# Kernel optimization log

Measured on AMD Instinct MI355X. Metric: run time of the kernel, lower is better.

Reference implementation:

```python
import jax, jax.numpy as jnp
import numpy as np

B, N, VDIM = 64, 256, 2048
LRDIM, EMBED = 64, 1024


def setup_inputs() -> dict:
    key = jax.random.key(0)
    ks = jax.random.split(key, 12)
    s = 1.0 / np.sqrt(VDIM)
    return {
        "Vmat": jax.random.normal(ks[0], (B, N, VDIM), dtype=jnp.float32),
        # weight-normed linear_U1: W = g * v / ||v||_row, bias b
        "U1_v": jax.random.normal(ks[1], (LRDIM, VDIM), dtype=jnp.float32) * s,
        "U1_g": jax.random.uniform(ks[2], (LRDIM,), dtype=jnp.float32, minval=0.5, maxval=1.5),
        "U1_b": jax.random.normal(ks[3], (LRDIM,), dtype=jnp.float32) * s,
        "U2_v": jax.random.normal(ks[4], (LRDIM, VDIM), dtype=jnp.float32) * s,
        "U2_g": jax.random.uniform(ks[5], (LRDIM,), dtype=jnp.float32, minval=0.5, maxval=1.5),
        "U2_b": jax.random.normal(ks[6], (LRDIM,), dtype=jnp.float32) * s,
        # final projection + BatchNorm1d affine params
        "W_lin": jax.random.normal(ks[7], (EMBED, VDIM), dtype=jnp.float32) * s,
        "b_lin": jax.random.normal(ks[8], (EMBED,), dtype=jnp.float32) * s,
        "bn_gamma": jnp.ones((EMBED,), dtype=jnp.float32),
        "bn_beta": jnp.zeros((EMBED,), dtype=jnp.float32),
    }


def _weight_norm(v, g):
    # torch weight_norm with dim=0: per output row
    return v * (g / jnp.linalg.norm(v, axis=1))[:, None]


def reference(Vmat, U1_v, U1_g, U1_b, U2_v, U2_g, U2_b, W_lin, b_lin, bn_gamma, bn_beta):
    # forward(Vmat, t_method='uncorr', model_num=6) -> UnCorrVmat_Detail path
    W1 = _weight_norm(U1_v, U1_g)
    W2 = _weight_norm(U2_v, U2_g)
    right = jax.nn.relu(jnp.einsum('bnv,kv->bnk', Vmat, W1) + U1_b)   # [B,N,LR]
    left = jax.nn.relu(jnp.einsum('bnv,kv->bnk', Vmat, W2) + U2_b)    # [B,N,LR]
    uncorr = jnp.einsum('bnk,bmk->bnm', left, right)                   # [B,N,N]
    # vectorized per-batch diag rsqrt normalization
    d = jax.lax.rsqrt(jnp.einsum('bii->bi', uncorr) + 1e-6)            # [B,N]
    uncorr = d[:, None, :] * uncorr * d[:, :, None]
    uncorr = 1.0 + jnp.eye(Vmat.shape[1], dtype=Vmat.dtype) - uncorr
    feats = jnp.mean(jnp.einsum('bnm,bmv->bnv', uncorr, Vmat), axis=1)  # [B,VDIM]
    # linear + BatchNorm1d (training mode: biased batch stats)
    x = feats @ W_lin.T + b_lin                                        # [B,EMBED]
    mu = jnp.mean(x, axis=0)
    var = jnp.mean(jnp.square(x - mu), axis=0)
    return bn_gamma * (x - mu) * jax.lax.rsqrt(var + 1e-5) + bn_beta
```

## Files before the change

kernel.cpp:

```cpp
#include <hip/hip_runtime.h>

#define B_ 64
#define N_ 256
#define V_ 2048
#define E_ 1024
#define MROWS 16384

typedef __bf16 bf16_t;
typedef bf16_t bf16x8 __attribute__((ext_vector_type(8)));
typedef float f32x4 __attribute__((ext_vector_type(4)));

#define OFF_LR  16384
#define OFF_FT  2113536
#define FTSZ    131072
#define OFF_WB  2637824

__device__ __forceinline__ void gload_lds16(const bf16_t* g, bf16_t* l) {
    __builtin_amdgcn_global_load_lds((const __attribute__((address_space(1))) void*)g,
                                     (__attribute__((address_space(3))) void*)l, 16, 0, 0);
}

__global__ void kprep(const float* __restrict__ U1v, const float* __restrict__ U1g,
                      const float* __restrict__ U2v, const float* __restrict__ U2g,
                      bf16_t* __restrict__ Wb) {
    __shared__ float red[256];
    __shared__ float sc;
    const int r = blockIdx.x;
    const float* v = (r < 64) ? (U1v + (size_t)r * V_) : (U2v + (size_t)(r - 64) * V_);
    float ss = 0.f;
    for (int i = threadIdx.x; i < V_; i += 256) { float x = v[i]; ss += x * x; }
    red[threadIdx.x] = ss;
    __syncthreads();
    for (int o = 128; o > 0; o >>= 1) {
        if (threadIdx.x < (unsigned)o) red[threadIdx.x] += red[threadIdx.x + o];
        __syncthreads();
    }
    if (threadIdx.x == 0) {
        float g = (r < 64) ? U1g[r] : U2g[r - 64];
        sc = g * rsqrtf(red[0]);
    }
    __syncthreads();
    const float s = sc;
    const int k = threadIdx.x * 8;
    float4 f0 = *(const float4*)(v + k);
    float4 f1 = *(const float4*)(v + k + 4);
    bf16x8 o;
    o[0] = (bf16_t)(f0.x * s); o[1] = (bf16_t)(f0.y * s);
    o[2] = (bf16_t)(f0.z * s); o[3] = (bf16_t)(f0.w * s);
    o[4] = (bf16_t)(f1.x * s); o[5] = (bf16_t)(f1.y * s);
    o[6] = (bf16_t)(f1.z * s); o[7] = (bf16_t)(f1.w * s);
    *(bf16x8*)(Wb + (size_t)r * V_ + k) = o;
}

#define BK 128
__global__ __launch_bounds__(256) void gemm_lr(
    const float* __restrict__ V, const bf16_t* __restrict__ Wb,
    const float* __restrict__ U1b, const float* __restrict__ U2b,
    float* __restrict__ LR) {
    __shared__ bf16_t As[32 * BK];
    __shared__ bf16_t Bs[128 * BK];
    const int t = threadIdx.x;
    const int m0 = blockIdx.x * 32;
    const int wv = t >> 6, lane = t & 63;
    const int lm = lane & 15, lq = lane >> 4;
    const int n0w = wv * 32;

    const int ar = t >> 3, au = t & 7;
    const float* aptr = V + (size_t)(m0 + ar) * V_ + au * 8;
    bf16_t* adst0 = &As[ar * BK + ((au ^ (ar & 15)) * 8)];
    bf16_t* adst1 = &As[ar * BK + (((au + 8) ^ (ar & 15)) * 8)];

    const int rloc = lane >> 4, cc = lane & 15;
    const int r15 = wv * 4 + rloc;
    const bf16_t* bgsrc = Wb + (size_t)r15 * V_ + (cc ^ r15) * 8;

    f32x4 acc[2][2];
#pragma unroll
    for (int i = 0; i < 2; ++i)
#pragma unroll
        for (int j = 0; j < 2; ++j) acc[i][j] = (f32x4){0.f, 0.f, 0.f, 0.f};

#pragma unroll
    for (int q = 0; q < 8; ++q)
        gload_lds16(bgsrc + (size_t)q * 16 * V_, &Bs[(q * 16 + wv * 4) * BK]);
    float4 ap0 = *(const float4*)(aptr);
    float4 ap1 = *(const float4*)(aptr + 4);
    float4 ap2 = *(const float4*)(aptr + 64);
    float4 ap3 = *(const float4*)(aptr + 68);

    for (int k0 = 0; k0 < V_; k0 += BK) {
        bf16x8 av0, av1;
        av0[0] = (bf16_t)ap0.x; av0[1] = (bf16_t)ap0.y; av0[2] = (bf16_t)ap0.z; av0[3] = (bf16_t)ap0.w;
        av0[4] = (bf16_t)ap1.x; av0[5] = (bf16_t)ap1.y; av0[6] = (bf16_t)ap1.z; av0[7] = (bf16_t)ap1.w;
        av1[0] = (bf16_t)ap2.x; av1[1] = (bf16_t)ap2.y; av1[2] = (bf16_t)ap2.z; av1[3] = (bf16_t)ap2.w;
        av1[4] = (bf16_t)ap3.x; av1[5] = (bf16_t)ap3.y; av1[6] = (bf16_t)ap3.z; av1[7] = (bf16_t)ap3.w;
        *(bf16x8*)adst0 = av0;
        *(bf16x8*)adst1 = av1;
        __syncthreads();

#pragma unroll
        for (int h = 0; h < 2; ++h) {
            bf16x8 af[2][2], bfr[2][2];
#pragma unroll
            for (int i = 0; i < 2; ++i)
#pragma unroll
                for (int kf = 0; kf < 2; ++kf)
                    af[i][kf] = *(bf16x8*)&As[(i * 16 + lm) * BK + ((((h * 2 + kf) * 4 + lq) ^ lm) * 8)];
#pragma unroll
            for (int j = 0; j < 2; ++j)
#pragma unroll
                for (int kf = 0; kf < 2; ++kf)
                    bfr[j][kf] = *(bf16x8*)&Bs[(n0w + j * 16 + lm) * BK + ((((h * 2 + kf) * 4 + lq) ^ lm) * 8)];
            if (h == 1 && k0 + BK < V_) {
                ap0 = *(const float4*)(aptr + k0 + BK);
                ap1 = *(const float4*)(aptr + k0 + BK + 4);
                ap2 = *(const float4*)(aptr + k0 + BK + 64);
                ap3 = *(const float4*)(aptr + k0 + BK + 68);
            }
#pragma unroll
            for (int i = 0; i < 2; ++i)
#pragma unroll
                for (int j = 0; j < 2; ++j) {
                    acc[i][j] = __builtin_amdgcn_mfma_f32_16x16x32_bf16(af[i][0], bfr[j][0], acc[i][j], 0, 0, 0);
                    acc[i][j] = __builtin_amdgcn_mfma_f32_16x16x32_bf16(af[i][1], bfr[j][1], acc[i][j], 0, 0, 0);
                }
        }
        __syncthreads();
        if (k0 + BK < V_) {
#pragma unroll
            for (int q = 0; q < 8; ++q)
                gload_lds16(bgsrc + (size_t)q * 16 * V_ + (k0 + BK), &Bs[(q * 16 + wv * 4) * BK]);
        }
    }
#pragma unroll
    for (int j = 0; j < 2; ++j) {
        const int n = n0w + j * 16 + lm;
        const float bi = (n < 64) ? U1b[n] : U2b[n - 64];
#pragma unroll
        for (int i = 0; i < 2; ++i)
#pragma unroll
            for (int r = 0; r < 4; ++r) {
                const int m = m0 + i * 16 + lq * 4 + r;
                LR[(size_t)m * 128 + n] = fmaxf(acc[i][j][r] + bi, 0.f);
            }
    }
}

__global__ __launch_bounds__(256) void kfs(const float* __restrict__ LR,
                                           const float* __restrict__ Vmat,
                                           float* __restrict__ F) {
    const int b = blockIdx.x >> 2, vc = blockIdx.x & 3;
    const float* Lb = LR + (size_t)b * N_ * 128;
    __shared__ float dl[256];
    __shared__ float red[4][64];
    __shared__ float lbar[64];
    __shared__ float sl[256];
    __shared__ float4 part[256];
    const int t = threadIdx.x;
    const float* row = Lb + (size_t)t * 128;
    float dd = 0.f;
#pragma unroll
    for (int k = 0; k < 64; k += 4) {
        float4 l = *(const float4*)(row + k);
        float4 r = *(const float4*)(row + 64 + k);
        dd += l.x * r.x + l.y * r.y + l.z * r.z + l.w * r.w;
    }
    const float dv = rsqrtf(dd + 1e-6f);
    dl[t] = dv;
    __syncthreads();
    const int k = t & 63, g = t >> 6;
    float acc = 0.f;
    for (int n = g; n < N_; n += 4)
        acc += dl[n] * Lb[(size_t)n * 128 + 64 + k];
    red[g][k] = acc;
    __syncthreads();
    if (t < 64) lbar[t] = red[0][t] + red[1][t] + red[2][t] + red[3][t];
    __syncthreads();
    float a2 = 0.f;
#pragma unroll 8
    for (int kk = 0; kk < 64; ++kk) a2 += lbar[kk] * row[kk];
    sl[t] = ((float)(N_ + 1) - dv * a2) * (1.0f / (float)N_);
    __syncthreads();
    const int v4 = t & 127, mh = t >> 7;
    const int v = vc * 512 + v4 * 4;
    const float* base = Vmat + (size_t)b * N_ * V_ + (size_t)mh * 128 * V_ + v;
    float4 a = {0.f, 0.f, 0.f, 0.f};
    for (int m = 0; m < 128; m += 16) {
        float4 x[16];
#pragma unroll
        for (int u = 0; u < 16; ++u) x[u] = *(const float4*)(base + (size_t)(m + u) * V_);
#pragma unroll
        for (int u = 0; u < 16; ++u) {
            float sv = sl[mh * 128 + m + u];
            a.x += sv * x[u].x; a.y += sv * x[u].y;
            a.z += sv * x[u].z; a.w += sv * x[u].w;
        }
    }
    part[t] = a;
    __syncthreads();
    if (mh == 0) {
        float4 p = part[t + 128];
        a = part[t];
        a.x += p.x; a.y += p.y; a.z += p.z; a.w += p.w;
        F[(size_t)(v + 0) * 64 + b] = a.x;
        F[(size_t)(v + 1) * 64 + b] = a.y;
        F[(size_t)(v + 2) * 64 + b] = a.z;
        F[(size_t)(v + 3) * 64 + b] = a.w;
    }
}

__global__ __launch_bounds__(512) void klinbn(const float* __restrict__ F,
                                              const float* __restrict__ Wl,
                                              const float* __restrict__ gamma,
                                              const float* __restrict__ beta,
                                              float* __restrict__ out) {
    __shared__ float red[8][4][64];
    const int e0 = blockIdx.x * 4;
    const int t = threadIdx.x, b = t & 63, g = t >> 6;
    const float* w0 = Wl + (size_t)(e0 + 0) * V_ + g * 256;
    const float* w1 = Wl + (size_t)(e0 + 1) * V_ + g * 256;
    const float* w2 = Wl + (size_t)(e0 + 2) * V_ + g * 256;
    const float* w3 = Wl + (size_t)(e0 + 3) * V_ + g * 256;
    const float* f0 = F + (size_t)g * 256 * 64 + b;
    float a0 = 0.f, a1 = 0.f, a2 = 0.f, a3 = 0.f;
#pragma unroll 4
    for (int k = 0; k < 256; ++k) {
        float fv = f0[(size_t)k * 64];
        a0 += fv * w0[k]; a1 += fv * w1[k]; a2 += fv * w2[k]; a3 += fv * w3[k];
    }
    red[g][0][b] = a0; red[g][1][b] = a1; red[g][2][b] = a2; red[g][3][b] = a3;
    __syncthreads();
    if (t < 256) {
        const int e = t >> 6;
        float v = 0.f;
#pragma unroll
        for (int gg = 0; gg < 8; ++gg) v += red[gg][e][b];
        float sum = v;
#pragma unroll
        for (int o = 1; o < 64; o <<= 1) sum += __shfl_xor(sum, o, 64);
        float mu = sum * (1.f / 64.f);
        float dvv = v - mu;
        float q = dvv * dvv;
#pragma unroll
        for (int o = 1; o < 64; o <<= 1) q += __shfl_xor(q, o, 64);
        float inv = rsqrtf(q * (1.f / 64.f) + 1e-5f);
        red[0][e][b] = gamma[e0 + e] * dvv * inv + beta[e0 + e];
    }
    __syncthreads();
    if (t < 256) {
        const int b2 = t >> 2, j = t & 3;
        out[(size_t)b2 * E_ + e0 + j] = red[0][j][b2];
    }
}

extern "C" void kernel_launch(void* const* d_in, const int* in_sizes, int n_in,
                              void* d_out, int out_size, void* d_ws, size_t ws_size,
                              hipStream_t stream) {
    const float* Vmat = (const float*)d_in[0];
    const float* U1v  = (const float*)d_in[1];
    const float* U1g  = (const float*)d_in[2];
    const float* U1b  = (const float*)d_in[3];
    const float* U2v  = (const float*)d_in[4];
    const float* U2g  = (const float*)d_in[5];
    const float* U2b  = (const float*)d_in[6];
    const float* Wl   = (const float*)d_in[7];
    const float* gam  = (const float*)d_in[9];
    const float* bet  = (const float*)d_in[10];

    float*  ws     = (float*)d_ws;
    float*  LR     = ws + OFF_LR;
    float*  F      = ws + OFF_FT;
    bf16_t* Wb     = (bf16_t*)(ws + OFF_WB);

    kprep  <<<128, 256, 0, stream>>>(U1v, U1g, U2v, U2g, Wb);
    gemm_lr<<<MROWS / 32, 256, 0, stream>>>(Vmat, Wb, U1b, U2b, LR);
    kfs    <<<B_ * 4, 256, 0, stream>>>(LR, Vmat, F);
    klinbn <<<E_ / 4, 512, 0, stream>>>(F, Wl, gam, bet, (float*)d_out);
}
```

Before: 280.1 us.

## Fuse all four stages into one cooperative persistent kernel with grid syncs

Replaces four separate launches (weight prep, low-rank GEMM, feature reduction, linear+BN) with a single cooperative kernel of 256 blocks that uses grid-wide syncs between stages. Each block handles 64 rows of the GEMM, with block ids mapped so that the rows a block computes belong to the batch it later reduces. This is meant to cut launch gaps and keep Vmat and LR rows in the same XCD's L2. In exchange the GEMM runs on only 256 blocks, doing two tiles each, instead of 512. Grid syncs add overhead, and the larger shared-memory footprint may lower occupancy.

```diff
diff --git a/kernel.cpp b/kernel.cpp
--- a/kernel.cpp
+++ b/kernel.cpp
@@ -1,10 +1,12 @@
 #include <hip/hip_runtime.h>
+#include <hip/hip_cooperative_groups.h>
+
+namespace cg = cooperative_groups;
 
 #define B_ 64
 #define N_ 256
 #define V_ 2048
 #define E_ 1024
-#define MROWS 16384
 
 typedef __bf16 bf16_t;
 typedef bf16_t bf16x8 __attribute__((ext_vector_type(8)));
@@ -12,244 +14,247 @@
 
 #define OFF_LR  16384
 #define OFF_FT  2113536
-#define FTSZ    131072
 #define OFF_WB  2637824
+#define BK 128
 
 __device__ __forceinline__ void gload_lds16(const bf16_t* g, bf16_t* l) {
     __builtin_amdgcn_global_load_lds((const __attribute__((address_space(1))) void*)g,
                                      (__attribute__((address_space(3))) void*)l, 16, 0, 0);
 }
 
-__global__ void kprep(const float* __restrict__ U1v, const float* __restrict__ U1g,
-                      const float* __restrict__ U2v, const float* __restrict__ U2g,
-                      bf16_t* __restrict__ Wb) {
-    __shared__ float red[256];
-    __shared__ float sc;
-    const int r = blockIdx.x;
-    const float* v = (r < 64) ? (U1v + (size_t)r * V_) : (U2v + (size_t)(r - 64) * V_);
-    float ss = 0.f;
-    for (int i = threadIdx.x; i < V_; i += 256) { float x = v[i]; ss += x * x; }
-    red[threadIdx.x] = ss;
-    __syncthreads();
-    for (int o = 128; o > 0; o >>= 1) {
-        if (threadIdx.x < (unsigned)o) red[threadIdx.x] += red[threadIdx.x + o];
-        __syncthreads();
-    }
-    if (threadIdx.x == 0) {
-        float g = (r < 64) ? U1g[r] : U2g[r - 64];
-        sc = g * rsqrtf(red[0]);
-    }
-    __syncthreads();
-    const float s = sc;
-    const int k = threadIdx.x * 8;
-    float4 f0 = *(const float4*)(v + k);
-    float4 f1 = *(const float4*)(v + k + 4);
-    bf16x8 o;
-    o[0] = (bf16_t)(f0.x * s); o[1] = (bf16_t)(f0.y * s);
-    o[2] = (bf16_t)(f0.z * s); o[3] = (bf16_t)(f0.w * s);
-    o[4] = (bf16_t)(f1.x * s); o[5] = (bf16_t)(f1.y * s);
-    o[6] = (bf16_t)(f1.z * s); o[7] = (bf16_t)(f1.w * s);
-    *(bf16x8*)(Wb + (size_t)r * V_ + k) = o;
-}
-
-#define BK 128
-__global__ __launch_bounds__(256) void gemm_lr(
-    const float* __restrict__ V, const bf16_t* __restrict__ Wb,
-    const float* __restrict__ U1b, const float* __restrict__ U2b,
-    float* __restrict__ LR) {
+__global__ __launch_bounds__(256) void kmega(
+    const float* __restrict__ Vmat,
+    const float* __restrict__ U1v, const float* __restrict__ U1g, const float* __restrict__ U1b,
+    const float* __restrict__ U2v, const float* __restrict__ U2g, const float* __restrict__ U2b,
+    const float* __restrict__ Wl, const float* __restrict__ gam, const float* __restrict__ bet,
+    float* __restrict__ LR, float* __restrict__ F, bf16_t* __restrict__ Wb,
+    float* __restrict__ out)
+{
+    cg::grid_group grid = cg::this_grid();
+    const int blk = blockIdx.x;
+    const int t = threadIdx.x;
+
     __shared__ bf16_t As[32 * BK];
     __shared__ bf16_t Bs[128 * BK];
-    const int t = threadIdx.x;
-    const int m0 = blockIdx.x * 32;
-    const int wv = t >> 6, lane = t & 63;
-    const int lm = lane & 15, lq = lane >> 4;
-    const int n0w = wv * 32;
-
-    const int ar = t >> 3, au = t & 7;
-    const float* aptr = V + (size_t)(m0 + ar) * V_ + au * 8;
-    bf16_t* adst0 = &As[ar * BK + ((au ^ (ar & 15)) * 8)];
-    bf16_t* adst1 = &As[ar * BK + (((au + 8) ^ (ar & 15)) * 8)];
-
-    const int rloc = lane >> 4, cc = lane & 15;
-    const int r15 = wv * 4 + rloc;
-    const bf16_t* bgsrc = Wb + (size_t)r15 * V_ + (cc ^ r15) * 8;
-
-    f32x4 acc[2][2];
-#pragma unroll
-    for (int i = 0; i < 2; ++i)
-#pragma unroll
-        for (int j = 0; j < 2; ++j) acc[i][j] = (f32x4){0.f, 0.f, 0.f, 0.f};
-
-#pragma unroll
-    for (int q = 0; q < 8; ++q)
-        gload_lds16(bgsrc + (size_t)q * 16 * V_, &Bs[(q * 16 + wv * 4) * BK]);
-    float4 ap0 = *(const float4*)(aptr);
-    float4 ap1 = *(const float4*)(aptr + 4);
-    float4 ap2 = *(const float4*)(aptr + 64);
-    float4 ap3 = *(const float4*)(aptr + 68);
-
-    for (int k0 = 0; k0 < V_; k0 += BK) {
-        bf16x8 av0, av1;
-        av0[0] = (bf16_t)ap0.x; av0[1] = (bf16_t)ap0.y; av0[2] = (bf16_t)ap0.z; av0[3] = (bf16_t)ap0.w;
-        av0[4] = (bf16_t)ap1.x; av0[5] = (bf16_t)ap1.y; av0[6] = (bf16_t)ap1.z; av0[7] = (bf16_t)ap1.w;
-        av1[0] = (bf16_t)ap2.x; av1[1] = (bf16_t)ap2.y; av1[2] = (bf16_t)ap2.z; av1[3] = (bf16_t)ap2.w;
-        av1[4] = (bf16_t)ap3.x; av1[5] = (bf16_t)ap3.y; av1[6] = (bf16_t)ap3.z; av1[7] = (bf16_t)ap3.w;
-        *(bf16x8*)adst0 = av0;
-        *(bf16x8*)adst1 = av1;
-        __syncthreads();
-
-#pragma unroll
-        for (int h = 0; h < 2; ++h) {
-            bf16x8 af[2][2], bfr[2][2];
-#pragma unroll
-            for (int i = 0; i < 2; ++i)
-#pragma unroll
-                for (int kf = 0; kf < 2; ++kf)
-                    af[i][kf] = *(bf16x8*)&As[(i * 16 + lm) * BK + ((((h * 2 + kf) * 4 + lq) ^ lm) * 8)];
-#pragma unroll
-            for (int j = 0; j < 2; ++j)
-#pragma unroll
-                for (int kf = 0; kf < 2; ++kf)
-                    bfr[j][kf] = *(bf16x8*)&Bs[(n0w + j * 16 + lm) * BK + ((((h * 2 + kf) * 4 + lq) ^ lm) * 8)];
-            if (h == 1 && k0 + BK < V_) {
-                ap0 = *(const float4*)(aptr + k0 + BK);
-                ap1 = *(const float4*)(aptr + k0 + BK + 4);
-                ap2 = *(const float4*)(aptr + k0 + BK + 64);
-                ap3 = *(const float4*)(aptr + k0 + BK + 68);
-            }
-#pragma unroll
-            for (int i = 0; i < 2; ++i)
-#pragma unroll
-                for (int j = 0; j < 2; ++j) {
-                    acc[i][j] = __builtin_amdgcn_mfma_f32_16x16x32_bf16(af[i][0], bfr[j][0], acc[i][j], 0, 0, 0);
-                    acc[i][j] = __builtin_amdgcn_mfma_f32_16x16x32_bf16(af[i][1], bfr[j][1], acc[i][j], 0, 0, 0);
-                }
-        }
-        __syncthreads();
-        if (k0 + BK < V_) {
-#pragma unroll
-            for (int q = 0; q < 8; ++q)
-                gload_lds16(bgsrc + (size_t)q * 16 * V_ + (k0 + BK), &Bs[(q * 16 + wv * 4) * BK]);
-        }
-    }
-#pragma unroll
-    for (int j = 0; j < 2; ++j) {
-        const int n = n0w + j * 16 + lm;
-        const float bi = (n < 64) ? U1b[n] : U2b[n - 64];
-#pragma unroll
-        for (int i = 0; i < 2; ++i)
-#pragma unroll
-            for (int r = 0; r < 4; ++r) {
-                const int m = m0 + i * 16 + lq * 4 + r;
-                LR[(size_t)m * 128 + n] = fmaxf(acc[i][j][r] + bi, 0.f);
-            }
-    }
-}
-
-__global__ __launch_bounds__(256) void kfs(const float* __restrict__ LR,
-                                           const float* __restrict__ Vmat,
-                                           float* __restrict__ F) {
-    const int b = blockIdx.x >> 2, vc = blockIdx.x & 3;
-    const float* Lb = LR + (size_t)b * N_ * 128;
+    __shared__ float pr_red[256];
+    __shared__ float pr_sc;
     __shared__ float dl[256];
-    __shared__ float red[4][64];
+    __shared__ float kred[4][64];
     __shared__ float lbar[64];
     __shared__ float sl[256];
     __shared__ float4 part[256];
-    const int t = threadIdx.x;
-    const float* row = Lb + (size_t)t * 128;
-    float dd = 0.f;
-#pragma unroll
-    for (int k = 0; k < 64; k += 4) {
-        float4 l = *(const float4*)(row + k);
-        float4 r = *(const float4*)(row + 64 + k);
-        dd += l.x * r.x + l.y * r.y + l.z * r.z + l.w * r.w;
-    }
-    const float dv = rsqrtf(dd + 1e-6f);
-    dl[t] = dv;
-    __syncthreads();
-    const int k = t & 63, g = t >> 6;
-    float acc = 0.f;
-    for (int n = g; n < N_; n += 4)
-        acc += dl[n] * Lb[(size_t)n * 128 + 64 + k];
-    red[g][k] = acc;
-    __syncthreads();
-    if (t < 64) lbar[t] = red[0][t] + red[1][t] + red[2][t] + red[3][t];
-    __syncthreads();
-    float a2 = 0.f;
+    __shared__ float lred[4][4][64];
+
+    const int xcd = blk & 7, slot = blk >> 3;
+    const int batch = xcd * 8 + (slot >> 2);
+    const int vcc = slot & 3;
+
+    if (blk < 128) {
+        const int r = blk;
+        const float* v = (r < 64) ? (U1v + (size_t)r * V_) : (U2v + (size_t)(r - 64) * V_);
+        float ss = 0.f;
+        for (int i = t; i < V_; i += 256) { float x = v[i]; ss += x * x; }
+        pr_red[t] = ss;
+        __syncthreads();
+        for (int o = 128; o > 0; o >>= 1) {
+            if (t < (unsigned)o) pr_red[t] += pr_red[t + o];
+            __syncthreads();
+        }
+        if (t == 0) {
+            float g = (r < 64) ? U1g[r] : U2g[r - 64];
+            pr_sc = g * rsqrtf(pr_red[0]);
+        }
+        __syncthreads();
+        const float s = pr_sc;
+        const int k = t * 8;
+        float4 f0 = *(const float4*)(v + k);
+        float4 f1 = *(const float4*)(v + k + 4);
+        bf16x8 o;
+        o[0] = (bf16_t)(f0.x * s); o[1] = (bf16_t)(f0.y * s);
+        o[2] = (bf16_t)(f0.z * s); o[3] = (bf16_t)(f0.w * s);
+        o[4] = (bf16_t)(f1.x * s); o[5] = (bf16_t)(f1.y * s);
+        o[6] = (bf16_t)(f1.z * s); o[7] = (bf16_t)(f1.w * s);
+        *(bf16x8*)(Wb + (size_t)r * V_ + k) = o;
+    }
+    grid.sync();
+
+    {
+        const int wv = t >> 6, lane = t & 63;
+        const int lm = lane & 15, lq = lane >> 4;
+        const int n0w = wv * 32;
+        const int ar = t >> 3, au = t & 7;
+        bf16_t* adst0 = &As[ar * BK + ((au ^ (ar & 15)) * 8)];
+        bf16_t* adst1 = &As[ar * BK + (((au + 8) ^ (ar & 15)) * 8)];
+        const int rloc = lane >> 4, cc = lane & 15;
+        const int r15 = wv * 4 + rloc;
+        const bf16_t* bgsrc = Wb + (size_t)r15 * V_ + (cc ^ r15) * 8;
+        const int base_m = batch * 256 + vcc * 64;
+
+        for (int tp = 0; tp < 2; ++tp) {
+            const int m0 = base_m + tp * 32;
+            const float* aptr = Vmat + (size_t)(m0 + ar) * V_ + au * 8;
+
+            f32x4 acc[2][2];
+#pragma unroll
+            for (int i = 0; i < 2; ++i)
+#pragma unroll
+                for (int j = 0; j < 2; ++j) acc[i][j] = (f32x4){0.f, 0.f, 0.f, 0.f};
+
+#pragma unroll
+            for (int q = 0; q < 8; ++q)
+                gload_lds16(bgsrc + (size_t)q * 16 * V_, &Bs[(q * 16 + wv * 4) * BK]);
+            float4 ap0 = *(const float4*)(aptr);
+            float4 ap1 = *(const float4*)(aptr + 4);
+            float4 ap2 = *(const float4*)(aptr + 64);
+            float4 ap3 = *(const float4*)(aptr + 68);
+
+            for (int k0 = 0; k0 < V_; k0 += BK) {
+                bf16x8 av0, av1;
+                av0[0] = (bf16_t)ap0.x; av0[1] = (bf16_t)ap0.y; av0[2] = (bf16_t)ap0.z; av0[3] = (bf16_t)ap0.w;
+                av0[4] = (bf16_t)ap1.x; av0[5] = (bf16_t)ap1.y; av0[6] = (bf16_t)ap1.z; av0[7] = (bf16_t)ap1.w;
+                av1[0] = (bf16_t)ap2.x; av1[1] = (bf16_t)ap2.y; av1[2] = (bf16_t)ap2.z; av1[3] = (bf16_t)ap2.w;
+                av1[4] = (bf16_t)ap3.x; av1[5] = (bf16_t)ap3.y; av1[6] = (bf16_t)ap3.z; av1[7] = (bf16_t)ap3.w;
+                *(bf16x8*)adst0 = av0;
+                *(bf16x8*)adst1 = av1;
+                __syncthreads();
+
+#pragma unroll
+                for (int h = 0; h < 2; ++h) {
+                    bf16x8 af[2][2], bfr[2][2];
+#pragma unroll
+                    for (int i = 0; i < 2; ++i)
+#pragma unroll
+                        for (int kf = 0; kf < 2; ++kf)
+                            af[i][kf] = *(bf16x8*)&As[(i * 16 + lm) * BK + ((((h * 2 + kf) * 4 + lq) ^ lm) * 8)];
+#pragma unroll
+                    for (int j = 0; j < 2; ++j)
+#pragma unroll
+                        for (int kf = 0; kf < 2; ++kf)
+                            bfr[j][kf] = *(bf16x8*)&Bs[(n0w + j * 16 + lm) * BK + ((((h * 2 + kf) * 4 + lq) ^ lm) * 8)];
+                    if (h == 1 && k0 + BK < V_) {
+                        ap0 = *(const float4*)(aptr + k0 + BK);
+                        ap1 = *(const float4*)(aptr + k0 + BK + 4);
+                        ap2 = *(const float4*)(aptr + k0 + BK + 64);
+                        ap3 = *(const float4*)(aptr + k0 + BK + 68);
+                    }
+#pragma unroll
+                    for (int i = 0; i < 2; ++i)
+#pragma unroll
+                        for (int j = 0; j < 2; ++j) {
+                            acc[i][j] = __builtin_amdgcn_mfma_f32_16x16x32_bf16(af[i][0], bfr[j][0], acc[i][j], 0, 0, 0);
+                            acc[i][j] = __builtin_amdgcn_mfma_f32_16x16x32_bf16(af[i][1], bfr[j][1], acc[i][j], 0, 0, 0);
+                        }
+                }
+                __syncthreads();
+                if (k0 + BK < V_) {
+#pragma unroll
+                    for (int q = 0; q < 8; ++q)
+                        gload_lds16(bgsrc + (size_t)q * 16 * V_ + (k0 + BK), &Bs[(q * 16 + wv * 4) * BK]);
+                }
+            }
+#pragma unroll
+            for (int j = 0; j < 2; ++j) {
+                const int n = n0w + j * 16 + lm;
+                const float bi = (n < 64) ? U1b[n] : U2b[n - 64];
+#pragma unroll
+                for (int i = 0; i < 2; ++i)
+#pragma unroll
+                    for (int r = 0; r < 4; ++r) {
+                        const int m = m0 + i * 16 + lq * 4 + r;
+                        LR[(size_t)m * 128 + n] = fmaxf(acc[i][j][r] + bi, 0.f);
+                    }
+            }
+        }
+    }
+    grid.sync();
+
+    {
+        const int b = batch, vc = vcc;
+        const float* Lb = LR + (size_t)b * N_ * 128;
+        const float* row = Lb + (size_t)t * 128;
+        float dd = 0.f;
+#pragma unroll
+        for (int k = 0; k < 64; k += 4) {
+            float4 l = *(const float4*)(row + k);
+            float4 r = *(const float4*)(row + 64 + k);
+            dd += l.x * r.x + l.y * r.y + l.z * r.z + l.w * r.w;
+        }
+        const float dv = rsqrtf(dd + 1e-6f);
+        dl[t] = dv;
+        __syncthreads();
+        const int k = t & 63, g = t >> 6;
+        float acc = 0.f;
+        for (int n = g; n < N_; n += 4)
+            acc += dl[n] * Lb[(size_t)n * 128 + 64 + k];
+        kred[g][k] = acc;
+        __syncthreads();
+        if (t < 64) lbar[t] = kred[0][t] + kred[1][t] + kred[2][t] + kred[3][t];
+        __syncthreads();
+        float a2 = 0.f;
 #pragma unroll 8
-    for (int kk = 0; kk < 64; ++kk) a2 += lbar[kk] * row[kk];
-    sl[t] = ((float)(N_ + 1) - dv * a2) * (1.0f / (float)N_);
-    __syncthreads();
-    const int v4 = t & 127, mh = t >> 7;
-    const int v = vc * 512 + v4 * 4;
-    const float* base = Vmat + (size_t)b * N_ * V_ + (size_t)mh * 128 * V_ + v;
-    float4 a = {0.f, 0.f, 0.f, 0.f};
-    for (int m = 0; m < 128; m += 16) {
-        float4 x[16];
-#pragma unroll
-        for (int u = 0; u < 16; ++u) x[u] = *(const float4*)(base + (size_t)(m + u) * V_);
-#pragma unroll
-        for (int u = 0; u < 16; ++u) {
-            float sv = sl[mh * 128 + m + u];
-            a.x += sv * x[u].x; a.y += sv * x[u].y;
-            a.z += sv * x[u].z; a.w += sv * x[u].w;
-        }
-    }
-    part[t] = a;
-    __syncthreads();
-    if (mh == 0) {
-        float4 p = part[t + 128];
-        a = part[t];
-        a.x += p.x; a.y += p.y; a.z += p.z; a.w += p.w;
-        F[(size_t)(v + 0) * 64 + b] = a.x;
-        F[(size_t)(v + 1) * 64 + b] = a.y;
-        F[(size_t)(v + 2) * 64 + b] = a.z;
-        F[(size_t)(v + 3) * 64 + b] = a.w;
-    }
-}
-
-__global__ __launch_bounds__(512) void klinbn(const float* __restrict__ F,
-                                              const float* __restrict__ Wl,
-                                              const float* __restrict__ gamma,
-                                              const float* __restrict__ beta,
-                                              float* __restrict__ out) {
-    __shared__ float red[8][4][64];
-    const int e0 = blockIdx.x * 4;
-    const int t = threadIdx.x, b = t & 63, g = t >> 6;
-    const float* w0 = Wl + (size_t)(e0 + 0) * V_ + g * 256;
-    const float* w1 = Wl + (size_t)(e0 + 1) * V_ + g * 256;
-    const float* w2 = Wl + (size_t)(e0 + 2) * V_ + g * 256;
-    const float* w3 = Wl + (size_t)(e0 + 3) * V_ + g * 256;
-    const float* f0 = F + (size_t)g * 256 * 64 + b;
-    float a0 = 0.f, a1 = 0.f, a2 = 0.f, a3 = 0.f;
+        for (int kk = 0; kk < 64; ++kk) a2 += lbar[kk] * row[kk];
+        sl[t] = ((float)(N_ + 1) - dv * a2) * (1.0f / (float)N_);
+        __syncthreads();
+        const int v4 = t & 127, mh = t >> 7;
+        const int v = vc * 512 + v4 * 4;
+        const float* base = Vmat + (size_t)b * N_ * V_ + (size_t)mh * 128 * V_ + v;
+        float4 a = {0.f, 0.f, 0.f, 0.f};
+        for (int m = 0; m < 128; m += 16) {
+            float4 x[16];
+#pragma unroll
+            for (int u = 0; u < 16; ++u) x[u] = *(const float4*)(base + (size_t)(m + u) * V_);
+#pragma unroll
+            for (int u = 0; u < 16; ++u) {
+                float sv = sl[mh * 128 + m + u];
+                a.x += sv * x[u].x; a.y += sv * x[u].y;
+                a.z += sv * x[u].z; a.w += sv * x[u].w;
+            }
+        }
+        part[t] = a;
+        __syncthreads();
+        if (mh == 0) {
+            float4 p = part[t + 128];
+            a = part[t];
+            a.x += p.x; a.y += p.y; a.z += p.z; a.w += p.w;
+            F[(size_t)(v + 0) * 64 + b] = a.x;
+            F[(size_t)(v + 1) * 64 + b] = a.y;
+            F[(size_t)(v + 2) * 64 + b] = a.z;
+            F[(size_t)(v + 3) * 64 + b] = a.w;
+        }
+    }
+    grid.sync();
+
+    {
+        const int e0 = blk * 4;
+        const int b = t & 63, g4 = t >> 6;
+        const float* w0 = Wl + (size_t)(e0 + 0) * V_ + g4 * 512;
+        const float* w1 = Wl + (size_t)(e0 + 1) * V_ + g4 * 512;
+        const float* w2 = Wl + (size_t)(e0 + 2) * V_ + g4 * 512;
+        const float* w3 = Wl + (size_t)(e0 + 3) * V_ + g4 * 512;
+        const float* f0 = F + (size_t)g4 * 512 * 64 + b;
+        float a0 = 0.f, a1 = 0.f, a2 = 0.f, a3 = 0.f;
 #pragma unroll 4
-    for (int k = 0; k < 256; ++k) {
-        float fv = f0[(size_t)k * 64];
-        a0 += fv * w0[k]; a1 += fv * w1[k]; a2 += fv * w2[k]; a3 += fv * w3[k];
-    }
-    red[g][0][b] = a0; red[g][1][b] = a1; red[g][2][b] = a2; red[g][3][b] = a3;
-    __syncthreads();
-    if (t < 256) {
+        for (int kk = 0; kk < 512; ++kk) {
+            float fv = f0[(size_t)kk * 64];
+            a0 += fv * w0[kk]; a1 += fv * w1[kk]; a2 += fv * w2[kk]; a3 += fv * w3[kk];
+        }
+        lred[g4][0][b] = a0; lred[g4][1][b] = a1; lred[g4][2][b] = a2; lred[g4][3][b] = a3;
+        __syncthreads();
         const int e = t >> 6;
-        float v = 0.f;
-#pragma unroll
-        for (int gg = 0; gg < 8; ++gg) v += red[gg][e][b];
-        float sum = v;
+        float vv = lred[0][e][b] + lred[1][e][b] + lred[2][e][b] + lred[3][e][b];
+        float sum = vv;
 #pragma unroll
         for (int o = 1; o < 64; o <<= 1) sum += __shfl_xor(sum, o, 64);
         float mu = sum * (1.f / 64.f);
-        float dvv = v - mu;
+        float dvv = vv - mu;
         float q = dvv * dvv;
 #pragma unroll
         for (int o = 1; o < 64; o <<= 1) q += __shfl_xor(q, o, 64);
         float inv = rsqrtf(q * (1.f / 64.f) + 1e-5f);
-        red[0][e][b] = gamma[e0 + e] * dvv * inv + beta[e0 + e];
-    }
-    __syncthreads();
-    if (t < 256) {
+        lred[0][e][b] = gam[e0 + e] * dvv * inv + bet[e0 + e];
+        __syncthreads();
         const int b2 = t >> 2, j = t & 3;
-        out[(size_t)b2 * E_ + e0 + j] = red[0][j][b2];
+        out[(size_t)b2 * E_ + e0 + j] = lred[0][j][b2];
     }
 }
 
@@ -267,13 +272,15 @@
     const float* gam  = (const float*)d_in[9];
     const float* bet  = (const float*)d_in[10];
 
-    float*  ws     = (float*)d_ws;
-    float*  LR     = ws + OFF_LR;
-    float*  F      = ws + OFF_FT;
-    bf16_t* Wb     = (bf16_t*)(ws + OFF_WB);
-
-    kprep  <<<128, 256, 0, stream>>>(U1v, U1g, U2v, U2g, Wb);
-    gemm_lr<<<MROWS / 32, 256, 0, stream>>>(Vmat, Wb, U1b, U2b, LR);
-    kfs    <<<B_ * 4, 256, 0, stream>>>(LR, Vmat, F);
-    klinbn <<<E_ / 4, 512, 0, stream>>>(F, Wl, gam, bet, (float*)d_out);
+    float*  ws   = (float*)d_ws;
+    float*  LRp  = ws + OFF_LR;
+    float*  Fp   = ws + OFF_FT;
+    bf16_t* Wbp  = (bf16_t*)(ws + OFF_WB);
+    float*  outp = (float*)d_out;
+
+    void* args[] = {(void*)&Vmat, (void*)&U1v, (void*)&U1g, (void*)&U1b,
+                    (void*)&U2v, (void*)&U2g, (void*)&U2b,
+                    (void*)&Wl, (void*)&gam, (void*)&bet,
+                    (void*)&LRp, (void*)&Fp, (void*)&Wbp, (void*)&outp};
+    hipLaunchCooperativeKernel((void*)kmega, dim3(256), dim3(256), args, 0, stream);
 }
```

New measurement: 418.3 us. 49.3% more time.

## Widen kfs to 1024 threads, splitting the row reduction eight ways

Applied to the files above, without the earlier changes.

Raises the kfs block size from 256 to 1024 threads while keeping 256 blocks. Each thread now streams 32 rows of Vmat instead of 128, and eight partial sums are reduced through shared memory. The aim is more memory-level parallelism, so the 128 MB Vmat read is spread over more waves on the 256 CUs. In exchange, three quarters of the threads sit idle during the per-row diag and scale phases, and shared memory use rises for the partial-sum buffer.

```diff
diff --git a/kernel.cpp b/kernel.cpp
--- a/kernel.cpp
+++ b/kernel.cpp
@@ -12,7 +12,6 @@
 
 #define OFF_LR  16384
 #define OFF_FT  2113536
-#define FTSZ    131072
 #define OFF_WB  2637824
 
 __device__ __forceinline__ void gload_lds16(const bf16_t* g, bf16_t* l) {
@@ -146,62 +145,77 @@
     }
 }
 
-__global__ __launch_bounds__(256) void kfs(const float* __restrict__ LR,
-                                           const float* __restrict__ Vmat,
-                                           float* __restrict__ F) {
+__global__ __launch_bounds__(1024) void kfs(const float* __restrict__ LR,
+                                            const float* __restrict__ Vmat,
+                                            float* __restrict__ F) {
     const int b = blockIdx.x >> 2, vc = blockIdx.x & 3;
     const float* Lb = LR + (size_t)b * N_ * 128;
     __shared__ float dl[256];
-    __shared__ float red[4][64];
+    __shared__ float kred[16][64];
     __shared__ float lbar[64];
     __shared__ float sl[256];
-    __shared__ float4 part[256];
+    __shared__ float4 part[1024];
     const int t = threadIdx.x;
-    const float* row = Lb + (size_t)t * 128;
-    float dd = 0.f;
-#pragma unroll
-    for (int k = 0; k < 64; k += 4) {
-        float4 l = *(const float4*)(row + k);
-        float4 r = *(const float4*)(row + 64 + k);
-        dd += l.x * r.x + l.y * r.y + l.z * r.z + l.w * r.w;
-    }
-    const float dv = rsqrtf(dd + 1e-6f);
-    dl[t] = dv;
-    __syncthreads();
-    const int k = t & 63, g = t >> 6;
-    float acc = 0.f;
-    for (int n = g; n < N_; n += 4)
-        acc += dl[n] * Lb[(size_t)n * 128 + 64 + k];
-    red[g][k] = acc;
-    __syncthreads();
-    if (t < 64) lbar[t] = red[0][t] + red[1][t] + red[2][t] + red[3][t];
-    __syncthreads();
-    float a2 = 0.f;
+
+    const float* row = Lb + (size_t)(t & 255) * 128;
+    if (t < 256) {
+        float dd = 0.f;
+#pragma unroll
+        for (int k = 0; k < 64; k += 4) {
+            float4 l = *(const float4*)(row + k);
+            float4 r = *(const float4*)(row + 64 + k);
+            dd += l.x * r.x + l.y * r.y + l.z * r.z + l.w * r.w;
+        }
+        dl[t] = rsqrtf(dd + 1e-6f);
+    }
+    __syncthreads();
+    {
+        const int k = t & 63, g = t >> 6;
+        float acc = 0.f;
+        for (int n = g; n < N_; n += 16)
+            acc += dl[n] * Lb[(size_t)n * 128 + 64 + k];
+        kred[g][k] = acc;
+    }
+    __syncthreads();
+    if (t < 64) {
+        float v = 0.f;
+#pragma unroll
+        for (int g = 0; g < 16; ++g) v += kred[g][t];
+        lbar[t] = v;
+    }
+    __syncthreads();
+    if (t < 256) {
+        float a2 = 0.f;
 #pragma unroll 8
-    for (int kk = 0; kk < 64; ++kk) a2 += lbar[kk] * row[kk];
-    sl[t] = ((float)(N_ + 1) - dv * a2) * (1.0f / (float)N_);
+        for (int kk = 0; kk < 64; ++kk) a2 += lbar[kk] * row[kk];
+        sl[t] = ((float)(N_ + 1) - dl[t] * a2) * (1.0f / (float)N_);
+    }
     __syncthreads();
     const int v4 = t & 127, mh = t >> 7;
     const int v = vc * 512 + v4 * 4;
-    const float* base = Vmat + (size_t)b * N_ * V_ + (size_t)mh * 128 * V_ + v;
+    const float* base = Vmat + (size_t)b * N_ * V_ + (size_t)mh * 32 * V_ + v;
     float4 a = {0.f, 0.f, 0.f, 0.f};
-    for (int m = 0; m < 128; m += 16) {
+#pragma unroll
+    for (int m = 0; m < 32; m += 16) {
         float4 x[16];
 #pragma unroll
         for (int u = 0; u < 16; ++u) x[u] = *(const float4*)(base + (size_t)(m + u) * V_);
 #pragma unroll
         for (int u = 0; u < 16; ++u) {
-            float sv = sl[mh * 128 + m + u];
+            float sv = sl[mh * 32 + m + u];
             a.x += sv * x[u].x; a.y += sv * x[u].y;
             a.z += sv * x[u].z; a.w += sv * x[u].w;
         }
     }
     part[t] = a;
     __syncthreads();
-    if (mh == 0) {
-        float4 p = part[t + 128];
+    if (t < 128) {
         a = part[t];
-        a.x += p.x; a.y += p.y; a.z += p.z; a.w += p.w;
+#pragma unroll
+        for (int g = 1; g < 8; ++g) {
+            float4 p = part[t + g * 128];
+            a.x += p.x; a.y += p.y; a.z += p.z; a.w += p.w;
+        }
         F[(size_t)(v + 0) * 64 + b] = a.x;
         F[(size_t)(v + 1) * 64 + b] = a.y;
         F[(size_t)(v + 2) * 64 + b] = a.z;
@@ -274,6 +288,6 @@
 
     kprep  <<<128, 256, 0, stream>>>(U1v, U1g, U2v, U2g, Wb);
     gemm_lr<<<MROWS / 32, 256, 0, stream>>>(Vmat, Wb, U1b, U2b, LR);
-    kfs    <<<B_ * 4, 256, 0, stream>>>(LR, Vmat, F);
+    kfs    <<<B_ * 4, 1024, 0, stream>>>(LR, Vmat, F);
     klinbn <<<E_ / 4, 512, 0, stream>>>(F, Wl, gam, bet, (float*)d_out);
 }
```

Result: no change. 277.2 us (-1.0%).
